# Kernel tuning notes

Measured on AMD Instinct MI355X. Metric: run time of the kernel, lower is better.

Reference implementation:

```python
import jax, jax.numpy as jnp
import numpy as np

N, E, F_IN, HID, EDIM, OUT = 50000, 800000, 128, 128, 32, 1
NEG_SLOPE = 0.2


def setup_inputs() -> dict:
    key = jax.random.key(0)
    ks = jax.random.split(key, 24)
    sc = 0.05
    d = {}
    d["x"] = jax.random.normal(ks[0], (N, F_IN), jnp.float32)
    d["src"] = jax.random.randint(ks[1], (E,), 0, N)
    d["dst"] = jax.random.randint(ks[2], (E,), 0, N)
    d["edge_attr"] = jax.random.normal(ks[3], (E, EDIM), jnp.float32)
    # conv1 params (GATConv(F_IN -> HID, edge_dim=EDIM), heads=1)
    d["W1"] = jax.random.normal(ks[4], (F_IN, HID), jnp.float32) * sc
    d["We1"] = jax.random.normal(ks[5], (EDIM, HID), jnp.float32) * sc
    d["as1"] = jax.random.normal(ks[6], (HID,), jnp.float32) * sc
    d["ad1"] = jax.random.normal(ks[7], (HID,), jnp.float32) * sc
    d["ae1"] = jax.random.normal(ks[8], (HID,), jnp.float32) * sc
    d["b1"] = jnp.zeros((HID,), jnp.float32)
    # conv2 params (GATConv(HID -> HID, edge_dim=EDIM))
    d["W2"] = jax.random.normal(ks[9], (HID, HID), jnp.float32) * sc
    d["We2"] = jax.random.normal(ks[10], (EDIM, HID), jnp.float32) * sc
    d["as2"] = jax.random.normal(ks[11], (HID,), jnp.float32) * sc
    d["ad2"] = jax.random.normal(ks[12], (HID,), jnp.float32) * sc
    d["ae2"] = jax.random.normal(ks[13], (HID,), jnp.float32) * sc
    d["b2"] = jnp.zeros((HID,), jnp.float32)
    # final linear
    d["Wl"] = jax.random.normal(ks[14], (HID, OUT), jnp.float32) * sc
    d["bl"] = jnp.zeros((OUT,), jnp.float32)
    return d


def _gat_conv(x, src, dst, e_attr, W, We, a_s, a_d, a_e, b):
    # x: [N, Fin], src/dst: [Et], e_attr: [Et, EDIM]
    h = x @ W                      # [N, C]
    ee = e_attr @ We               # [Et, C]
    alpha = h @ a_s                # per-node source logit [N]
    beta = h @ a_d                 # per-node dest logit   [N]
    logit = alpha[src] + beta[dst] + ee @ a_e          # [Et]
    logit = jax.nn.leaky_relu(logit, NEG_SLOPE)
    # segment softmax over destination node
    m = jax.ops.segment_max(logit, dst, num_segments=N)
    ex = jnp.exp(logit - m[dst])
    s = jax.ops.segment_sum(ex, dst, num_segments=N)
    w = ex / (s[dst] + 1e-16)                          # [Et]
    out = jax.ops.segment_sum(h[src] * w[:, None], dst, num_segments=N)
    return out + b


def reference(x, src, dst, edge_attr, W1, We1, as1, ad1, ae1, b1,
              W2, We2, as2, ad2, ae2, b2, Wl, bl):
    # add_self_loops=True with fill_value='mean' (PyG GATConv default)
    loop = jnp.arange(N, dtype=src.dtype)
    src2 = jnp.concatenate([src, loop])
    dst2 = jnp.concatenate([dst, loop])
    mean_ea = jnp.mean(edge_attr, axis=0)
    ea2 = jnp.concatenate([edge_attr, jnp.broadcast_to(mean_ea, (N, EDIM))], axis=0)
    h = _gat_conv(x, src2, dst2, ea2, W1, We1, as1, ad1, ae1, b1)
    h = jax.nn.relu(h)                 # dropout is identity in eval mode
    h = _gat_conv(h, src2, dst2, ea2, W2, We2, as2, ad2, ae2, b2)
    out = h @ Wl + bl
    return jax.nn.relu(out)            # [N, 1]
```

## Files before the change

kernel.cpp:

```cpp
#include <hip/hip_runtime.h>
#include <math.h>

#define N_NODES 50000
#define N_EDGES 800000
#define HIDDEN  128
#define EDIM    32
#define NEG     0.2f

typedef __attribute__((ext_vector_type(8))) short bshort8;
typedef __attribute__((ext_vector_type(4))) float f32x4;

__device__ __forceinline__ unsigned short f2bf(float f) {
    unsigned u = __builtin_bit_cast(unsigned, f);
    return (unsigned short)((u + 0x7FFFu + ((u >> 16) & 1u)) >> 16);
}
__device__ __forceinline__ float bf2f(unsigned short b) {
    unsigned u = ((unsigned)b) << 16;
    return __builtin_bit_cast(float, u);
}

#define TILES_M (N_NODES / 16)
#define GEMM_BLOCKS ((TILES_M + 3) / 4)
#define EB (N_EDGES / 256)
#define SCAN_BLOCKS ((N_NODES + 255) / 256)

#define X_SPLIT 35008
#define TILES_SPLIT (X_SPLIT / 16)
#define AGG_B1 (X_SPLIT / 4)
#define AGG_B2 ((N_NODES - X_SPLIT) / 4)
#define GEMM_B2 ((TILES_SPLIT + 3) / 4)
#define GEMM_B3 ((TILES_M - TILES_SPLIT + 3) / 4)

__device__ __forceinline__ void pack_w_body(int idx, const float* __restrict__ W,
                                            unsigned short* __restrict__ whp,
                                            unsigned short* __restrict__ wlp) {
    int e  = idx & 7;
    int l  = (idx >> 3) & 63;
    int kc = (idx >> 9) & 3;
    int ct = (idx >> 11);
    int k   = kc * 32 + ((l >> 4) << 3) + e;
    int col = ct * 16 + (l & 15);
    float w = W[k * HIDDEN + col];
    unsigned short hb = f2bf(w);
    whp[idx] = hb;
    wlp[idx] = f2bf(w - bf2f(hb));
}

template<int MODE>
__device__ __forceinline__ void gemm_body(int tile, int t,
                                          const float* __restrict__ x,
                                          const unsigned short* __restrict__ wh,
                                          const unsigned short* __restrict__ wl,
                                          const float* __restrict__ a_s,
                                          const float* __restrict__ a_d,
                                          const float* __restrict__ gv,
                                          float* __restrict__ h,
                                          float* __restrict__ alpha,
                                          float* __restrict__ beta,
                                          float2* __restrict__ pg) {
    int l    = t & 63;
    int row0 = tile * 16;
    int arow = l & 15;
    int kg   = l >> 4;
    bshort8 ah[4], al[4];
    const float* xr = x + (size_t)(row0 + arow) * HIDDEN + (kg << 3);
#pragma unroll
    for (int kc = 0; kc < 4; kc++) {
        float4 f0 = *(const float4*)(xr + kc * 32);
        float4 f1 = *(const float4*)(xr + kc * 32 + 4);
        float fv[8] = {f0.x, f0.y, f0.z, f0.w, f1.x, f1.y, f1.z, f1.w};
#pragma unroll
        for (int e = 0; e < 8; e++) {
            unsigned short hb = f2bf(fv[e]);
            ah[kc][e] = (short)hb;
            al[kc][e] = (short)f2bf(fv[e] - bf2f(hb));
        }
    }
    float pal[4] = {0.f, 0.f, 0.f, 0.f};
    float pbe[4] = {0.f, 0.f, 0.f, 0.f};
    float pgl[4] = {0.f, 0.f, 0.f, 0.f};
#pragma unroll
    for (int ct = 0; ct < 8; ct++) {
        f32x4 acc = {0.f, 0.f, 0.f, 0.f};
#pragma unroll
        for (int kc = 0; kc < 4; kc++) {
            int fo = (((ct * 4 + kc) * 64) + l) << 3;
            bshort8 bh = *(const bshort8*)(wh + fo);
            bshort8 bl = *(const bshort8*)(wl + fo);
            acc = __builtin_amdgcn_mfma_f32_16x16x32_bf16(ah[kc], bh, acc, 0, 0, 0);
            acc = __builtin_amdgcn_mfma_f32_16x16x32_bf16(al[kc], bh, acc, 0, 0, 0);
            acc = __builtin_amdgcn_mfma_f32_16x16x32_bf16(ah[kc], bl, acc, 0, 0, 0);
        }
        int col = ct * 16 + arow;
        float a_sc = a_s[col], a_dc = a_d[col];
        float gvc = (MODE == 1) ? gv[col] : 0.f;
#pragma unroll
        for (int j = 0; j < 4; j++) {
            if (MODE == 0)
                h[(size_t)(row0 + kg * 4 + j) * HIDDEN + col] = acc[j];
            pal[j] += acc[j] * a_sc;
            pbe[j] += acc[j] * a_dc;
            if (MODE == 1) pgl[j] += acc[j] * gvc;
        }
    }
#pragma unroll
    for (int m = 1; m < 16; m <<= 1) {
#pragma unroll
        for (int j = 0; j < 4; j++) {
            pal[j] += __shfl_xor(pal[j], m, 64);
            pbe[j] += __shfl_xor(pbe[j], m, 64);
            if (MODE == 1) pgl[j] += __shfl_xor(pgl[j], m, 64);
        }
    }
    if (arow == 0) {
#pragma unroll
        for (int j = 0; j < 4; j++) {
            int r = row0 + kg * 4 + j;
            if (MODE == 0) {
                alpha[r] = pal[j];
                beta[r]  = pbe[j];
            } else {
                beta[r] = pbe[j];
                pg[r]   = make_float2(pal[j], pgl[j]);
            }
        }
    }
}

__device__ __forceinline__ void agg_body(int i, int t,
                                         const int* __restrict__ off_work,
                                         const int* __restrict__ blockoff,
                                         const int* __restrict__ count,
                                         const float4* __restrict__ erec,
                                         const float* __restrict__ h,
                                         const float* __restrict__ alpha,
                                         const float* __restrict__ beta,
                                         const float* __restrict__ b,
                                         const float* __restrict__ part,
                                         float* __restrict__ outp) {
    int l = t & 63;
    float ps = part[l * 16];
#pragma unroll
    for (int m = 32; m > 0; m >>= 1) ps += __shfl_xor(ps, m, 64);
    float selfc = ps * (1.f / (float)N_EDGES);
    int start = off_work[i] + blockoff[i >> 8];
    int end   = start + count[i];
    float beta_i = beta[i];
    float2 acc = make_float2(0.f, 0.f);
    float wsum = 0.f;
    for (int cb = start; cb < end; cb += 64) {
        int n = min(64, end - cb);
        int sp = 0; float wt = 0.f;
        if (l < n) {
            float4 rec = erec[cb + l];
            sp = __float_as_int(rec.z);
            float lg = alpha[sp] + beta_i + rec.x;
            lg = lg > 0.f ? lg : NEG * lg;
            wt = expf(lg);
        }
        int j = 0;
        for (; j + 8 <= n; j += 8) {
            float w8[8]; int s8[8]; float2 h8[8];
#pragma unroll
            for (int q = 0; q < 8; q++) {
                w8[q] = __shfl(wt, j + q, 64);
                s8[q] = __shfl(sp, j + q, 64);
            }
#pragma unroll
            for (int q = 0; q < 8; q++)
                h8[q] = ((const float2*)(h + (size_t)s8[q] * HIDDEN))[l];
#pragma unroll
            for (int q = 0; q < 8; q++) {
                acc.x += w8[q] * h8[q].x;
                acc.y += w8[q] * h8[q].y;
                wsum  += w8[q];
            }
        }
        for (; j + 4 <= n; j += 4) {
            float w4[4]; int s4[4]; float2 h4[4];
#pragma unroll
            for (int q = 0; q < 4; q++) {
                w4[q] = __shfl(wt, j + q, 64);
                s4[q] = __shfl(sp, j + q, 64);
            }
#pragma unroll
            for (int q = 0; q < 4; q++)
                h4[q] = ((const float2*)(h + (size_t)s4[q] * HIDDEN))[l];
#pragma unroll
            for (int q = 0; q < 4; q++) {
                acc.x += w4[q] * h4[q].x;
                acc.y += w4[q] * h4[q].y;
                wsum  += w4[q];
            }
        }
        for (; j < n; j++) {
            float w = __shfl(wt, j, 64);
            int   sj = __shfl(sp, j, 64);
            float2 hv = ((const float2*)(h + (size_t)sj * HIDDEN))[l];
            acc.x += w * hv.x;
            acc.y += w * hv.y;
            wsum  += w;
        }
    }
    float lg = alpha[i] + beta_i + selfc;
    lg = lg > 0.f ? lg : NEG * lg;
    float exi = expf(lg);
    float denom = wsum + exi + 1e-16f;
    float2 hv = ((const float2*)(h + (size_t)i * HIDDEN))[l];
    float2 bb = ((const float2*)b)[l];
    float2 v;
    v.x = (acc.x + exi * hv.x) / denom + bb.x;
    v.y = (acc.y + exi * hv.y) / denom + bb.y;
    ((float2*)(outp + (size_t)i * HIDDEN))[l] =
        make_float2(fmaxf(v.x, 0.f), fmaxf(v.y, 0.f));
}

__global__ void __launch_bounds__(256)
fused_prep_kernel(const int* __restrict__ dst, int* __restrict__ count,
                  int* __restrict__ rank,
                  const float* __restrict__ W1, unsigned short* __restrict__ whp1,
                  unsigned short* __restrict__ wlp1,
                  const float* __restrict__ W2, unsigned short* __restrict__ whp2,
                  unsigned short* __restrict__ wlp2,
                  const float* __restrict__ We1, const float* __restrict__ ae1,
                  const float* __restrict__ We2, const float* __restrict__ ae2,
                  const float* __restrict__ b2, const float* __restrict__ Wlin,
                  const float* __restrict__ bl, float* __restrict__ consts) {
    int b = blockIdx.x, t = threadIdx.x;
    if (b < EB) {
        int e = b * 256 + t;
        rank[e] = atomicAdd(&count[dst[e]], 1);
    } else if (b < EB + 64) {
        pack_w_body((b - EB) * 256 + t, W1, whp1, wlp1);
    } else if (b < EB + 128) {
        pack_w_body((b - EB - 64) * 256 + t, W2, whp2, wlp2);
    } else {
        if (t < 32) {
            float acc = 0.f;
            for (int k = 0; k < HIDDEN; k++) acc += We1[t * HIDDEN + k] * ae1[k];
            consts[t] = acc;
        } else if (t < 64) {
            int j = t - 32;
            float acc = 0.f;
            for (int k = 0; k < HIDDEN; k++) acc += We2[j * HIDDEN + k] * ae2[k];
            consts[32 + j] = acc;
        } else if (t < 128) {
            int k = t - 64;
            float p = b2[k] * Wlin[k] + b2[k + 64] * Wlin[k + 64];
            for (int off = 32; off > 0; off >>= 1) p += __shfl_down(p, off, 64);
            if (t == 64) consts[64] = p + bl[0];
        }
    }
}

__global__ void scan1_kernel(const int* __restrict__ count,
                             int* __restrict__ off_work, int* __restrict__ blocksum) {
    __shared__ int sh[256];
    int t = threadIdx.x;
    int idx = blockIdx.x * 256 + t;
    int v = (idx < N_NODES) ? count[idx] : 0;
    sh[t] = v;
    __syncthreads();
    for (int off = 1; off < 256; off <<= 1) {
        int u = (t >= off) ? sh[t - off] : 0;
        __syncthreads();
        sh[t] += u;
        __syncthreads();
    }
    if (idx < N_NODES) off_work[idx] = sh[t] - v;
    if (t == 255) blocksum[blockIdx.x] = sh[255];
}
__global__ void scan2_kernel(int* __restrict__ blocksum, int* __restrict__ blockoff) {
    __shared__ int sh[256];
    int t = threadIdx.x;
    int v = (t < SCAN_BLOCKS) ? blocksum[t] : 0;
    sh[t] = v;
    __syncthreads();
    for (int off = 1; off < 256; off <<= 1) {
        int u = (t >= off) ? sh[t - off] : 0;
        __syncthreads();
        sh[t] += u;
        __syncthreads();
    }
    if (t < SCAN_BLOCKS) blockoff[t] = sh[t] - v;
}

__global__ void __launch_bounds__(256)
fused_scatter_gemm_kernel(const int* __restrict__ src, const int* __restrict__ dst,
                          const int* __restrict__ rank,
                          const float* __restrict__ ea,
                          const float* __restrict__ consts,
                          const int* __restrict__ off_work,
                          const int* __restrict__ blockoff,
                          float4* __restrict__ erec, float* __restrict__ part,
                          const float* __restrict__ x,
                          const unsigned short* __restrict__ wh,
                          const unsigned short* __restrict__ wl,
                          const float* __restrict__ a_s, const float* __restrict__ a_d,
                          float* __restrict__ h, float* __restrict__ alpha,
                          float* __restrict__ beta) {
    __shared__ float cs[64];
    int b = blockIdx.x, t = threadIdx.x;
    bool is_gemm = ((b & 3) == 3) && ((b >> 2) < GEMM_BLOCKS);
    if (is_gemm) {
        int tile = (b >> 2) * 4 + (t >> 6);
        if (tile < TILES_M)
            gemm_body<0>(tile, t, x, wh, wl, a_s, a_d, nullptr, h, alpha, beta, nullptr);
        return;
    }
    int sid = b - min((b + 1) >> 2, GEMM_BLOCKS);
    if (t < 64) cs[t] = consts[t];
    __syncthreads();
    int e = sid * 256 + t;
    const float4* ep = (const float4*)(ea + (size_t)e * EDIM);
    float d1 = 0.f, d2 = 0.f;
#pragma unroll
    for (int i = 0; i < 8; i++) {
        float4 v = ep[i];
        d1 += v.x * cs[4 * i] + v.y * cs[4 * i + 1] + v.z * cs[4 * i + 2] + v.w * cs[4 * i + 3];
        d2 += v.x * cs[32 + 4 * i] + v.y * cs[32 + 4 * i + 1] + v.z * cs[32 + 4 * i + 2] + v.w * cs[32 + 4 * i + 3];
    }
    int d = dst[e];
    int pos = off_work[d] + blockoff[d >> 8] + rank[e];
    erec[pos] = make_float4(d1, d2, __int_as_float(src[e]), 0.f);
    float s1 = d1, s2 = d2;
    for (int off = 32; off > 0; off >>= 1) {
        s1 += __shfl_down(s1, off, 64);
        s2 += __shfl_down(s2, off, 64);
    }
    if ((t & 63) == 0) {
        int slot = (sid & 63) * 16;
        atomicAdd(&part[slot], s1);
        atomicAdd(&part[slot + 1], s2);
    }
}

__global__ void __launch_bounds__(256)
agg1_k1_kernel(const int* __restrict__ off_work, const int* __restrict__ blockoff,
               const int* __restrict__ count, const float4* __restrict__ erec,
               const float* __restrict__ h, const float* __restrict__ alpha,
               const float* __restrict__ beta, const float* __restrict__ b,
               const float* __restrict__ part, float* __restrict__ outp) {
    int i = blockIdx.x * 4 + (threadIdx.x >> 6);
    agg_body(i, threadIdx.x, off_work, blockoff, count, erec, h, alpha, beta,
             b, part, outp);
}

__global__ void __launch_bounds__(256)
fused_agg_gemm_kernel(const int* __restrict__ off_work, const int* __restrict__ blockoff,
                      const int* __restrict__ count, const float4* __restrict__ erec,
                      const float* __restrict__ h1, const float* __restrict__ alpha1,
                      const float* __restrict__ beta1, const float* __restrict__ b1,
                      const float* __restrict__ part, float* __restrict__ outB,
                      const float* __restrict__ Bx,
                      const unsigned short* __restrict__ wh2,
                      const unsigned short* __restrict__ wl2,
                      const float* __restrict__ as2, const float* __restrict__ ad2,
                      const float* __restrict__ Wlin,
                      float* __restrict__ beta2, float2* __restrict__ pg) {
    int b = blockIdx.x, t = threadIdx.x;
    bool is_gemm = ((b % 7) == 6) && ((b / 7) < GEMM_B2);
    if (is_gemm) {
        int tile = (b / 7) * 4 + (t >> 6);
        if (tile < TILES_SPLIT)
            gemm_body<1>(tile, t, Bx, wh2, wl2, as2, ad2, Wlin,
                         nullptr, nullptr, beta2, pg);
        return;
    }
    int sid = b - min((b + 1) / 7, GEMM_B2);
    int i = X_SPLIT + sid * 4 + (t >> 6);
    agg_body(i, t, off_work, blockoff, count, erec, h1, alpha1, beta1,
             b1, part, outB);
}

__global__ void __launch_bounds__(256)
gemm_k3_kernel(const float* __restrict__ Bx,
               const unsigned short* __restrict__ wh2,
               const unsigned short* __restrict__ wl2,
               const float* __restrict__ as2, const float* __restrict__ ad2,
               const float* __restrict__ Wlin,
               float* __restrict__ beta2, float2* __restrict__ pg) {
    int tile = TILES_SPLIT + blockIdx.x * 4 + (threadIdx.x >> 6);
    if (tile >= TILES_M) return;
    gemm_body<1>(tile, threadIdx.x, Bx, wh2, wl2, as2, ad2, Wlin,
                 nullptr, nullptr, beta2, pg);
}

__global__ void __launch_bounds__(256)
agg2_lite_kernel(const int* __restrict__ off_work, const int* __restrict__ blockoff,
                 const int* __restrict__ count, const float4* __restrict__ erec,
                 const float2* __restrict__ pg, const float* __restrict__ beta2,
                 const float* __restrict__ part, const float* __restrict__ consts,
                 float* __restrict__ out) {
    int t = threadIdx.x, l = t & 63;
    int i = blockIdx.x * 4 + (t >> 6);
    float ps = part[l * 16 + 1];
#pragma unroll
    for (int m = 32; m > 0; m >>= 1) ps += __shfl_xor(ps, m, 64);
    float selfc = ps * (1.f / (float)N_EDGES);
    int start = off_work[i] + blockoff[i >> 8];
    int end   = start + count[i];
    float beta_i = beta2[i];
    float wsum = 0.f, gsum = 0.f;
    for (int e = start + l; e < end; e += 64) {
        float4 rec = erec[e];
        int sp = __float_as_int(rec.z);
        float2 ag = pg[sp];
        float lg = ag.x + beta_i + rec.y;
        lg = lg > 0.f ? lg : NEG * lg;
        float w = expf(lg);
        wsum += w;
        gsum += w * ag.y;
    }
    for (int m = 32; m > 0; m >>= 1) {
        wsum += __shfl_xor(wsum, m, 64);
        gsum += __shfl_xor(gsum, m, 64);
    }
    if (l == 0) {
        float2 agi = pg[i];
        float lg = agi.x + beta_i + selfc;
        lg = lg > 0.f ? lg : NEG * lg;
        float exi = expf(lg);
        float denom = wsum + exi + 1e-16f;
        out[i] = fmaxf((gsum + exi * agi.y) / denom + consts[64], 0.f);
    }
}

extern "C" void kernel_launch(void* const* d_in, const int* in_sizes, int n_in,
                              void* d_out, int out_size, void* d_ws, size_t ws_size,
                              hipStream_t stream) {
    const float* x   = (const float*)d_in[0];
    const int*   src = (const int*)  d_in[1];
    const int*   dst = (const int*)  d_in[2];
    const float* ea  = (const float*)d_in[3];
    const float* W1  = (const float*)d_in[4];
    const float* We1 = (const float*)d_in[5];
    const float* as1 = (const float*)d_in[6];
    const float* ad1 = (const float*)d_in[7];
    const float* ae1 = (const float*)d_in[8];
    const float* b1  = (const float*)d_in[9];
    const float* W2  = (const float*)d_in[10];
    const float* We2 = (const float*)d_in[11];
    const float* as2 = (const float*)d_in[12];
    const float* ad2 = (const float*)d_in[13];
    const float* ae2 = (const float*)d_in[14];
    const float* b2  = (const float*)d_in[15];
    const float* Wl  = (const float*)d_in[16];
    const float* bl  = (const float*)d_in[17];
    float* out = (float*)d_out;

    float* ws      = (float*)d_ws;
    float* A       = ws;
    float* B       = A + (size_t)N_NODES * HIDDEN;
    float4* erec   = (float4*)(B + (size_t)N_NODES * HIDDEN);
    unsigned short* whp1 = (unsigned short*)(erec + N_EDGES);
    unsigned short* wlp1 = whp1 + 16384;
    unsigned short* whp2 = wlp1 + 16384;
    unsigned short* wlp2 = whp2 + 16384;
    float* alpha1  = (float*)(wlp2 + 16384);
    float* beta1   = alpha1 + N_NODES;
    float* beta2   = beta1 + N_NODES;
    float2* pg     = (float2*)(beta2 + N_NODES);
    float* consts  = (float*)(pg + N_NODES);
    float* part    = consts + 80;
    int* count     = (int*)(part + 64 * 16);
    int* off_work  = count + N_NODES;
    int* blocksum  = off_work + N_NODES;
    int* blockoff  = blocksum + SCAN_BLOCKS;
    int* rank      = blockoff + SCAN_BLOCKS;

    hipMemsetAsync(count, 0, N_NODES * sizeof(int), stream);
    hipMemsetAsync(part, 0, 64 * 16 * sizeof(float), stream);
    fused_prep_kernel<<<EB + 129, 256, 0, stream>>>(dst, count, rank,
                                                    W1, whp1, wlp1, W2, whp2, wlp2,
                                                    We1, ae1, We2, ae2,
                                                    b2, Wl, bl, consts);
    scan1_kernel<<<SCAN_BLOCKS, 256, 0, stream>>>(count, off_work, blocksum);
    scan2_kernel<<<1, 256, 0, stream>>>(blocksum, blockoff);

    fused_scatter_gemm_kernel<<<EB + GEMM_BLOCKS, 256, 0, stream>>>(
        src, dst, rank, ea, consts, off_work, blockoff, erec, part,
        x, whp1, wlp1, as1, ad1, A, alpha1, beta1);

    agg1_k1_kernel<<<AGG_B1, 256, 0, stream>>>(off_work, blockoff, count, erec,
                                               A, alpha1, beta1, b1, part, B);
    fused_agg_gemm_kernel<<<AGG_B2 + GEMM_B2, 256, 0, stream>>>(
        off_work, blockoff, count, erec, A, alpha1, beta1, b1, part, B,
        B, whp2, wlp2, as2, ad2, Wl, beta2, pg);
    gemm_k3_kernel<<<GEMM_B3, 256, 0, stream>>>(B, whp2, wlp2, as2, ad2,
                                                Wl, beta2, pg);

    agg2_lite_kernel<<<N_NODES / 4, 256, 0, stream>>>(off_work, blockoff, count,
                                                      erec, pg, beta2, part,
                                                      consts, out);
}
```

Before: 209.4 us.

## Fold layer-2 GEMM into aggregation via precomputed W2 projections

Layer 2 only needs three scalars per node (h2·a_s2, h2·a_d2, h2·Wl), so the prep kernel now precomputes W2·Wl, W2·as2 and W2·ad2 as 128-vectors. The first aggregation kernel dots its ReLU output row against these vectors and writes beta2 and pg directly. This removes the second MFMA GEMM, the W2 bf16 packing, the intermediate N×128 buffer B and two kernel launches. The cost is a few extra warp reductions per node in the aggregation and slightly different float rounding.

```diff
diff --git a/kernel.cpp b/kernel.cpp
--- a/kernel.cpp
+++ b/kernel.cpp
@@ -23,13 +23,6 @@
 #define GEMM_BLOCKS ((TILES_M + 3) / 4)
 #define EB (N_EDGES / 256)
 #define SCAN_BLOCKS ((N_NODES + 255) / 256)
-
-#define X_SPLIT 35008
-#define TILES_SPLIT (X_SPLIT / 16)
-#define AGG_B1 (X_SPLIT / 4)
-#define AGG_B2 ((N_NODES - X_SPLIT) / 4)
-#define GEMM_B2 ((TILES_SPLIT + 3) / 4)
-#define GEMM_B3 ((TILES_M - TILES_SPLIT + 3) / 4)
 
 __device__ __forceinline__ void pack_w_body(int idx, const float* __restrict__ W,
                                             unsigned short* __restrict__ whp,
@@ -46,18 +39,15 @@
     wlp[idx] = f2bf(w - bf2f(hb));
 }
 
-template<int MODE>
 __device__ __forceinline__ void gemm_body(int tile, int t,
                                           const float* __restrict__ x,
                                           const unsigned short* __restrict__ wh,
                                           const unsigned short* __restrict__ wl,
                                           const float* __restrict__ a_s,
                                           const float* __restrict__ a_d,
-                                          const float* __restrict__ gv,
                                           float* __restrict__ h,
                                           float* __restrict__ alpha,
-                                          float* __restrict__ beta,
-                                          float2* __restrict__ pg) {
+                                          float* __restrict__ beta) {
     int l    = t & 63;
     int row0 = tile * 16;
     int arow = l & 15;
@@ -78,7 +68,6 @@
     }
     float pal[4] = {0.f, 0.f, 0.f, 0.f};
     float pbe[4] = {0.f, 0.f, 0.f, 0.f};
-    float pgl[4] = {0.f, 0.f, 0.f, 0.f};
 #pragma unroll
     for (int ct = 0; ct < 8; ct++) {
         f32x4 acc = {0.f, 0.f, 0.f, 0.f};
@@ -93,14 +82,11 @@
         }
         int col = ct * 16 + arow;
         float a_sc = a_s[col], a_dc = a_d[col];
-        float gvc = (MODE == 1) ? gv[col] : 0.f;
 #pragma unroll
         for (int j = 0; j < 4; j++) {
-            if (MODE == 0)
-                h[(size_t)(row0 + kg * 4 + j) * HIDDEN + col] = acc[j];
+            h[(size_t)(row0 + kg * 4 + j) * HIDDEN + col] = acc[j];
             pal[j] += acc[j] * a_sc;
             pbe[j] += acc[j] * a_dc;
-            if (MODE == 1) pgl[j] += acc[j] * gvc;
         }
     }
 #pragma unroll
@@ -109,110 +95,15 @@
         for (int j = 0; j < 4; j++) {
             pal[j] += __shfl_xor(pal[j], m, 64);
             pbe[j] += __shfl_xor(pbe[j], m, 64);
-            if (MODE == 1) pgl[j] += __shfl_xor(pgl[j], m, 64);
         }
     }
     if (arow == 0) {
 #pragma unroll
         for (int j = 0; j < 4; j++) {
-            int r = row0 + kg * 4 + j;
-            if (MODE == 0) {
-                alpha[r] = pal[j];
-                beta[r]  = pbe[j];
-            } else {
-                beta[r] = pbe[j];
-                pg[r]   = make_float2(pal[j], pgl[j]);
-            }
-        }
-    }
-}
-
-__device__ __forceinline__ void agg_body(int i, int t,
-                                         const int* __restrict__ off_work,
-                                         const int* __restrict__ blockoff,
-                                         const int* __restrict__ count,
-                                         const float4* __restrict__ erec,
-                                         const float* __restrict__ h,
-                                         const float* __restrict__ alpha,
-                                         const float* __restrict__ beta,
-                                         const float* __restrict__ b,
-                                         const float* __restrict__ part,
-                                         float* __restrict__ outp) {
-    int l = t & 63;
-    float ps = part[l * 16];
-#pragma unroll
-    for (int m = 32; m > 0; m >>= 1) ps += __shfl_xor(ps, m, 64);
-    float selfc = ps * (1.f / (float)N_EDGES);
-    int start = off_work[i] + blockoff[i >> 8];
-    int end   = start + count[i];
-    float beta_i = beta[i];
-    float2 acc = make_float2(0.f, 0.f);
-    float wsum = 0.f;
-    for (int cb = start; cb < end; cb += 64) {
-        int n = min(64, end - cb);
-        int sp = 0; float wt = 0.f;
-        if (l < n) {
-            float4 rec = erec[cb + l];
-            sp = __float_as_int(rec.z);
-            float lg = alpha[sp] + beta_i + rec.x;
-            lg = lg > 0.f ? lg : NEG * lg;
-            wt = expf(lg);
-        }
-        int j = 0;
-        for (; j + 8 <= n; j += 8) {
-            float w8[8]; int s8[8]; float2 h8[8];
-#pragma unroll
-            for (int q = 0; q < 8; q++) {
-                w8[q] = __shfl(wt, j + q, 64);
-                s8[q] = __shfl(sp, j + q, 64);
-            }
-#pragma unroll
-            for (int q = 0; q < 8; q++)
-                h8[q] = ((const float2*)(h + (size_t)s8[q] * HIDDEN))[l];
-#pragma unroll
-            for (int q = 0; q < 8; q++) {
-                acc.x += w8[q] * h8[q].x;
-                acc.y += w8[q] * h8[q].y;
-                wsum  += w8[q];
-            }
-        }
-        for (; j + 4 <= n; j += 4) {
-            float w4[4]; int s4[4]; float2 h4[4];
-#pragma unroll
-            for (int q = 0; q < 4; q++) {
-                w4[q] = __shfl(wt, j + q, 64);
-                s4[q] = __shfl(sp, j + q, 64);
-            }
-#pragma unroll
-            for (int q = 0; q < 4; q++)
-                h4[q] = ((const float2*)(h + (size_t)s4[q] * HIDDEN))[l];
-#pragma unroll
-            for (int q = 0; q < 4; q++) {
-                acc.x += w4[q] * h4[q].x;
-                acc.y += w4[q] * h4[q].y;
-                wsum  += w4[q];
-            }
-        }
-        for (; j < n; j++) {
-            float w = __shfl(wt, j, 64);
-            int   sj = __shfl(sp, j, 64);
-            float2 hv = ((const float2*)(h + (size_t)sj * HIDDEN))[l];
-            acc.x += w * hv.x;
-            acc.y += w * hv.y;
-            wsum  += w;
-        }
-    }
-    float lg = alpha[i] + beta_i + selfc;
-    lg = lg > 0.f ? lg : NEG * lg;
-    float exi = expf(lg);
-    float denom = wsum + exi + 1e-16f;
-    float2 hv = ((const float2*)(h + (size_t)i * HIDDEN))[l];
-    float2 bb = ((const float2*)b)[l];
-    float2 v;
-    v.x = (acc.x + exi * hv.x) / denom + bb.x;
-    v.y = (acc.y + exi * hv.y) / denom + bb.y;
-    ((float2*)(outp + (size_t)i * HIDDEN))[l] =
-        make_float2(fmaxf(v.x, 0.f), fmaxf(v.y, 0.f));
+            alpha[row0 + kg * 4 + j] = pal[j];
+            beta[row0 + kg * 4 + j]  = pbe[j];
+        }
+    }
 }
 
 __global__ void __launch_bounds__(256)
@@ -220,10 +111,10 @@
                   int* __restrict__ rank,
                   const float* __restrict__ W1, unsigned short* __restrict__ whp1,
                   unsigned short* __restrict__ wlp1,
-                  const float* __restrict__ W2, unsigned short* __restrict__ whp2,
-                  unsigned short* __restrict__ wlp2,
                   const float* __restrict__ We1, const float* __restrict__ ae1,
                   const float* __restrict__ We2, const float* __restrict__ ae2,
+                  const float* __restrict__ W2,
+                  const float* __restrict__ as2, const float* __restrict__ ad2,
                   const float* __restrict__ b2, const float* __restrict__ Wlin,
                   const float* __restrict__ bl, float* __restrict__ consts) {
     int b = blockIdx.x, t = threadIdx.x;
@@ -232,9 +123,7 @@
         rank[e] = atomicAdd(&count[dst[e]], 1);
     } else if (b < EB + 64) {
         pack_w_body((b - EB) * 256 + t, W1, whp1, wlp1);
-    } else if (b < EB + 128) {
-        pack_w_body((b - EB - 64) * 256 + t, W2, whp2, wlp2);
-    } else {
+    } else if (b == EB + 64) {
         if (t < 32) {
             float acc = 0.f;
             for (int k = 0; k < HIDDEN; k++) acc += We1[t * HIDDEN + k] * ae1[k];
@@ -249,6 +138,20 @@
             float p = b2[k] * Wlin[k] + b2[k + 64] * Wlin[k + 64];
             for (int off = 32; off > 0; off >>= 1) p += __shfl_down(p, off, 64);
             if (t == 64) consts[64] = p + bl[0];
+        }
+    } else {
+        if (t < HIDDEN) {
+            const float* wr = W2 + (size_t)t * HIDDEN;
+            float su = 0.f, sa = 0.f, sb = 0.f;
+            for (int k = 0; k < HIDDEN; k++) {
+                float w = wr[k];
+                su += w * Wlin[k];
+                sa += w * as2[k];
+                sb += w * ad2[k];
+            }
+            consts[128 + t] = su;
+            consts[256 + t] = sa;
+            consts[384 + t] = sb;
         }
     }
 }
@@ -305,7 +208,7 @@
     if (is_gemm) {
         int tile = (b >> 2) * 4 + (t >> 6);
         if (tile < TILES_M)
-            gemm_body<0>(tile, t, x, wh, wl, a_s, a_d, nullptr, h, alpha, beta, nullptr);
+            gemm_body(tile, t, x, wh, wl, a_s, a_d, h, alpha, beta);
         return;
     }
     int sid = b - min((b + 1) >> 2, GEMM_BLOCKS);
@@ -336,54 +239,101 @@
 }
 
 __global__ void __launch_bounds__(256)
-agg1_k1_kernel(const int* __restrict__ off_work, const int* __restrict__ blockoff,
-               const int* __restrict__ count, const float4* __restrict__ erec,
-               const float* __restrict__ h, const float* __restrict__ alpha,
-               const float* __restrict__ beta, const float* __restrict__ b,
-               const float* __restrict__ part, float* __restrict__ outp) {
-    int i = blockIdx.x * 4 + (threadIdx.x >> 6);
-    agg_body(i, threadIdx.x, off_work, blockoff, count, erec, h, alpha, beta,
-             b, part, outp);
-}
-
-__global__ void __launch_bounds__(256)
-fused_agg_gemm_kernel(const int* __restrict__ off_work, const int* __restrict__ blockoff,
-                      const int* __restrict__ count, const float4* __restrict__ erec,
-                      const float* __restrict__ h1, const float* __restrict__ alpha1,
-                      const float* __restrict__ beta1, const float* __restrict__ b1,
-                      const float* __restrict__ part, float* __restrict__ outB,
-                      const float* __restrict__ Bx,
-                      const unsigned short* __restrict__ wh2,
-                      const unsigned short* __restrict__ wl2,
-                      const float* __restrict__ as2, const float* __restrict__ ad2,
-                      const float* __restrict__ Wlin,
-                      float* __restrict__ beta2, float2* __restrict__ pg) {
-    int b = blockIdx.x, t = threadIdx.x;
-    bool is_gemm = ((b % 7) == 6) && ((b / 7) < GEMM_B2);
-    if (is_gemm) {
-        int tile = (b / 7) * 4 + (t >> 6);
-        if (tile < TILES_SPLIT)
-            gemm_body<1>(tile, t, Bx, wh2, wl2, as2, ad2, Wlin,
-                         nullptr, nullptr, beta2, pg);
-        return;
-    }
-    int sid = b - min((b + 1) / 7, GEMM_B2);
-    int i = X_SPLIT + sid * 4 + (t >> 6);
-    agg_body(i, t, off_work, blockoff, count, erec, h1, alpha1, beta1,
-             b1, part, outB);
-}
-
-__global__ void __launch_bounds__(256)
-gemm_k3_kernel(const float* __restrict__ Bx,
-               const unsigned short* __restrict__ wh2,
-               const unsigned short* __restrict__ wl2,
-               const float* __restrict__ as2, const float* __restrict__ ad2,
-               const float* __restrict__ Wlin,
-               float* __restrict__ beta2, float2* __restrict__ pg) {
-    int tile = TILES_SPLIT + blockIdx.x * 4 + (threadIdx.x >> 6);
-    if (tile >= TILES_M) return;
-    gemm_body<1>(tile, threadIdx.x, Bx, wh2, wl2, as2, ad2, Wlin,
-                 nullptr, nullptr, beta2, pg);
+agg1_kernel(const int* __restrict__ off_work, const int* __restrict__ blockoff,
+            const int* __restrict__ count, const float4* __restrict__ erec,
+            const float* __restrict__ h,
+            const float* __restrict__ alpha, const float* __restrict__ beta,
+            const float* __restrict__ b, const float* __restrict__ part,
+            const float* __restrict__ consts,
+            float* __restrict__ beta2, float2* __restrict__ pg) {
+    int t = threadIdx.x;
+    int l = t & 63;
+    int i = blockIdx.x * 4 + (t >> 6);
+    float ps = part[l * 16];
+#pragma unroll
+    for (int m = 32; m > 0; m >>= 1) ps += __shfl_xor(ps, m, 64);
+    float selfc = ps * (1.f / (float)N_EDGES);
+    int start = off_work[i] + blockoff[i >> 8];
+    int end   = start + count[i];
+    float beta_i = beta[i];
+    float2 acc = make_float2(0.f, 0.f);
+    float wsum = 0.f;
+    for (int cb = start; cb < end; cb += 64) {
+        int n = min(64, end - cb);
+        int sp = 0; float wt = 0.f;
+        if (l < n) {
+            float4 rec = erec[cb + l];
+            sp = __float_as_int(rec.z);
+            float lg = alpha[sp] + beta_i + rec.x;
+            lg = lg > 0.f ? lg : NEG * lg;
+            wt = expf(lg);
+        }
+        int j = 0;
+        for (; j + 8 <= n; j += 8) {
+            float w8[8]; int s8[8]; float2 h8[8];
+#pragma unroll
+            for (int q = 0; q < 8; q++) {
+                w8[q] = __shfl(wt, j + q, 64);
+                s8[q] = __shfl(sp, j + q, 64);
+            }
+#pragma unroll
+            for (int q = 0; q < 8; q++)
+                h8[q] = ((const float2*)(h + (size_t)s8[q] * HIDDEN))[l];
+#pragma unroll
+            for (int q = 0; q < 8; q++) {
+                acc.x += w8[q] * h8[q].x;
+                acc.y += w8[q] * h8[q].y;
+                wsum  += w8[q];
+            }
+        }
+        for (; j + 4 <= n; j += 4) {
+            float w4[4]; int s4[4]; float2 h4[4];
+#pragma unroll
+            for (int q = 0; q < 4; q++) {
+                w4[q] = __shfl(wt, j + q, 64);
+                s4[q] = __shfl(sp, j + q, 64);
+            }
+#pragma unroll
+            for (int q = 0; q < 4; q++)
+                h4[q] = ((const float2*)(h + (size_t)s4[q] * HIDDEN))[l];
+#pragma unroll
+            for (int q = 0; q < 4; q++) {
+                acc.x += w4[q] * h4[q].x;
+                acc.y += w4[q] * h4[q].y;
+                wsum  += w4[q];
+            }
+        }
+        for (; j < n; j++) {
+            float w = __shfl(wt, j, 64);
+            int   sj = __shfl(sp, j, 64);
+            float2 hv = ((const float2*)(h + (size_t)sj * HIDDEN))[l];
+            acc.x += w * hv.x;
+            acc.y += w * hv.y;
+            wsum  += w;
+        }
+    }
+    float lg = alpha[i] + beta_i + selfc;
+    lg = lg > 0.f ? lg : NEG * lg;
+    float exi = expf(lg);
+    float denom = wsum + exi + 1e-16f;
+    float2 hv = ((const float2*)(h + (size_t)i * HIDDEN))[l];
+    float2 bb = ((const float2*)b)[l];
+    float bx = fmaxf((acc.x + exi * hv.x) / denom + bb.x, 0.f);
+    float by = fmaxf((acc.y + exi * hv.y) / denom + bb.y, 0.f);
+    int c0 = 2 * l, c1 = 2 * l + 1;
+    float pa2 = bx * consts[256 + c0] + by * consts[256 + c1];
+    float pb2 = bx * consts[384 + c0] + by * consts[384 + c1];
+    float pgv = bx * consts[128 + c0] + by * consts[128 + c1];
+#pragma unroll
+    for (int m = 32; m > 0; m >>= 1) {
+        pa2 += __shfl_xor(pa2, m, 64);
+        pb2 += __shfl_xor(pb2, m, 64);
+        pgv += __shfl_xor(pgv, m, 64);
+    }
+    if (l == 0) {
+        beta2[i] = pb2;
+        pg[i] = make_float2(pa2, pgv);
+    }
 }
 
 __global__ void __launch_bounds__(256)
@@ -451,18 +401,15 @@
 
     float* ws      = (float*)d_ws;
     float* A       = ws;
-    float* B       = A + (size_t)N_NODES * HIDDEN;
-    float4* erec   = (float4*)(B + (size_t)N_NODES * HIDDEN);
+    float4* erec   = (float4*)(A + (size_t)N_NODES * HIDDEN);
     unsigned short* whp1 = (unsigned short*)(erec + N_EDGES);
     unsigned short* wlp1 = whp1 + 16384;
-    unsigned short* whp2 = wlp1 + 16384;
-    unsigned short* wlp2 = whp2 + 16384;
-    float* alpha1  = (float*)(wlp2 + 16384);
+    float* alpha1  = (float*)(wlp1 + 16384);
     float* beta1   = alpha1 + N_NODES;
     float* beta2   = beta1 + N_NODES;
     float2* pg     = (float2*)(beta2 + N_NODES);
     float* consts  = (float*)(pg + N_NODES);
-    float* part    = consts + 80;
+    float* part    = consts + 512;
     int* count     = (int*)(part + 64 * 16);
     int* off_work  = count + N_NODES;
     int* blocksum  = off_work + N_NODES;
@@ -471,10 +418,11 @@
 
     hipMemsetAsync(count, 0, N_NODES * sizeof(int), stream);
     hipMemsetAsync(part, 0, 64 * 16 * sizeof(float), stream);
-    fused_prep_kernel<<<EB + 129, 256, 0, stream>>>(dst, count, rank,
-                                                    W1, whp1, wlp1, W2, whp2, wlp2,
-                                                    We1, ae1, We2, ae2,
-                                                    b2, Wl, bl, consts);
+    fused_prep_kernel<<<EB + 66, 256, 0, stream>>>(dst, count, rank,
+                                                   W1, whp1, wlp1,
+                                                   We1, ae1, We2, ae2,
+                                                   W2, as2, ad2, b2, Wl, bl,
+                                                   consts);
     scan1_kernel<<<SCAN_BLOCKS, 256, 0, stream>>>(count, off_work, blocksum);
     scan2_kernel<<<1, 256, 0, stream>>>(blocksum, blockoff);
 
@@ -482,13 +430,9 @@
         src, dst, rank, ea, consts, off_work, blockoff, erec, part,
         x, whp1, wlp1, as1, ad1, A, alpha1, beta1);
 
-    agg1_k1_kernel<<<AGG_B1, 256, 0, stream>>>(off_work, blockoff, count, erec,
-                                               A, alpha1, beta1, b1, part, B);
-    fused_agg_gemm_kernel<<<AGG_B2 + GEMM_B2, 256, 0, stream>>>(
-        off_work, blockoff, count, erec, A, alpha1, beta1, b1, part, B,
-        B, whp2, wlp2, as2, ad2, Wl, beta2, pg);
-    gemm_k3_kernel<<<GEMM_B3, 256, 0, stream>>>(B, whp2, wlp2, as2, ad2,
-                                                Wl, beta2, pg);
+    agg1_kernel<<<N_NODES / 4, 256, 0, stream>>>(off_work, blockoff, count, erec,
+                                                 A, alpha1, beta1, b1, part,
+                                                 consts, beta2, pg);
 
     agg2_lite_kernel<<<N_NODES / 4, 256, 0, stream>>>(off_work, blockoff, count,
                                                       erec, pg, beta2, part,
```

New measurement: 187.2 us, median of 2. 10.6% less time.
